# Performance work log

Measured on AMD Instinct MI355X. Metric: run time of the kernel, lower is better.

The kernel has to match this reference:

```python
import jax, jax.numpy as jnp
import numpy as np

HIDDEN = 128
BSZ, C, Q = 8, 512, 64


def setup_inputs() -> dict:
    key = jax.random.key(0)
    k1, k2, k3, k4 = jax.random.split(key, 4)
    h = jax.random.normal(k1, (BSZ, C, HIDDEN), dtype=jnp.float32)
    u = jax.random.normal(k2, (BSZ, Q, HIDDEN), dtype=jnp.float32)
    # torch Linear stores weight as (out, in); xavier-uniform-like init
    lim1 = float(np.sqrt(6.0 / (3 * HIDDEN + HIDDEN)))
    w1 = jax.random.uniform(k3, (HIDDEN, 3 * HIDDEN), jnp.float32, -lim1, lim1)
    b1 = jnp.zeros((HIDDEN,), jnp.float32)
    lim2 = float(np.sqrt(6.0 / (HIDDEN + 1)))
    w2 = jax.random.uniform(k4, (1, HIDDEN), jnp.float32, -lim2, lim2)
    b2 = jnp.zeros((1,), jnp.float32)
    return {"h": h, "u": u, "w1": w1, "b1": b1, "w2": w2, "b2": b2}


def reference(h, u, w1, b1, w2, b2):
    # Decompose l1 weight into blocks acting on [h2, u2, h2*u2] so the
    # (bsz, C, Q, 3*hidden) concat tensor is never materialized.
    hid = h.shape[-1]
    w_h, w_u, w_hu = w1[:, :hid], w1[:, hid:2 * hid], w1[:, 2 * hid:]
    h_proj = jnp.einsum('bcd,kd->bck', h, w_h)          # (b, C, hidden)
    u_proj = jnp.einsum('bqd,kd->bqk', u, w_u)          # (b, Q, hidden)
    hu_proj = jnp.einsum('bcd,bqd,kd->bcqk', h, u, w_hu)  # (b, C, Q, hidden)
    l1 = jax.nn.relu(h_proj[:, :, None, :] + u_proj[:, None, :, :] + hu_proj + b1)
    l2 = jax.nn.relu(jnp.einsum('bcqk,ok->bcqo', l1, w2) + b2)
    out = jnp.squeeze(l2, axis=-1)  # (b, C, Q)
    if out.ndim == 2:  # bsz == 1 case in original
        out = out[None]
    return out
```

## Files before the change

kernel.cpp:

```cpp
#include <hip/hip_runtime.h>
#include <hip/hip_bf16.h>

typedef __bf16 bf16;
typedef __bf16 bf16x4 __attribute__((ext_vector_type(4)));
typedef __bf16 bf16x8 __attribute__((ext_vector_type(8)));
typedef float  f32x4  __attribute__((ext_vector_type(4)));

#define HID   128
#define BSZ   8
#define CDIM  512
#define QDIM  64
#define LDH   136
#define CTILE 128

__global__ __launch_bounds__(256, 2)
void sim_kernel(const float* __restrict__ hptr,
                const float* __restrict__ uptr,
                const float* __restrict__ w1,
                const float* __restrict__ b1,
                const float* __restrict__ w2,
                const float* __restrict__ b2,
                float* __restrict__ out)
{
    __shared__ bf16  weff[HID * LDH];
    __shared__ bf16  hsh[CTILE * LDH];
    __shared__ float ush[HID];
    __shared__ float bias_sh[HID];
    __shared__ float w2sh[HID];

    const int t  = threadIdx.x;
    const int bi = blockIdx.x >> 6;
    const int qi = blockIdx.x & 63;

    const float* uvec = uptr + (bi * QDIM + qi) * HID;

    if (t < HID) {
        ush[t]  = uvec[t];
        w2sh[t] = w2[t];
    }
    __syncthreads();

    {
        const int k     = t >> 1;
        const int dbase = (t & 1) * 64;
        const float* wrow = w1 + k * 384;
        #pragma unroll
        for (int j = 0; j < 16; ++j) {
            const int d = dbase + j * 4;
            float4 wh  = *(const float4*)(wrow + d);
            float4 whu = *(const float4*)(wrow + 256 + d);
            bf16x4 o;
            o[0] = (bf16)(wh.x + ush[d + 0] * whu.x);
            o[1] = (bf16)(wh.y + ush[d + 1] * whu.y);
            o[2] = (bf16)(wh.z + ush[d + 2] * whu.z);
            o[3] = (bf16)(wh.w + ush[d + 3] * whu.w);
            *(bf16x4*)&weff[k * LDH + d] = o;
        }
    }
    if (t < HID) {
        const float* wrow = w1 + t * 384 + 128;
        float acc = 0.f;
        #pragma unroll 8
        for (int d = 0; d < 128; d += 4) {
            float4 wu = *(const float4*)(wrow + d);
            acc += wu.x * ush[d] + wu.y * ush[d + 1] + wu.z * ush[d + 2] + wu.w * ush[d + 3];
        }
        bias_sh[t] = b1[t] + acc;
    }
    __syncthreads();

    const int lane = t & 63;
    const int wv   = t >> 6;
    const int col  = lane & 15;
    const int quad = lane >> 4;

    bf16x8 bfrag[4][8];
    #pragma unroll
    for (int ks = 0; ks < 4; ++ks)
        #pragma unroll
        for (int n = 0; n < 8; ++n)
            bfrag[ks][n] = *(const bf16x8*)&weff[(n * 16 + col) * LDH + ks * 32 + quad * 8];

    float bias_l[8], w2_l[8];
    #pragma unroll
    for (int n = 0; n < 8; ++n) {
        bias_l[n] = bias_sh[n * 16 + col];
        w2_l[n]   = w2sh[n * 16 + col];
    }
    const float b2v = b2[0];

    const float* hbase = hptr + bi * (CDIM * HID);
    float*       obase = out + (bi * CDIM) * QDIM + qi;

    for (int ct = 0; ct < CDIM / CTILE; ++ct) {
        __syncthreads();
        {
            const int c0 = ct * CTILE;
            #pragma unroll
            for (int i = 0; i < 16; ++i) {
                const int flat4 = i * 256 + t;
                const int row   = flat4 >> 5;
                const int c4    = flat4 & 31;
                float4 v = *(const float4*)(hbase + (c0 + row) * HID + c4 * 4);
                bf16x4 o;
                o[0] = (bf16)v.x; o[1] = (bf16)v.y; o[2] = (bf16)v.z; o[3] = (bf16)v.w;
                *(bf16x4*)&hsh[row * LDH + c4 * 4] = o;
            }
        }
        __syncthreads();

        #pragma unroll
        for (int rt = 0; rt < 2; ++rt) {
            f32x4 acc[8];
            #pragma unroll
            for (int n = 0; n < 8; ++n) acc[n] = (f32x4){0.f, 0.f, 0.f, 0.f};

            #pragma unroll
            for (int ks = 0; ks < 4; ++ks) {
                bf16x8 a = *(const bf16x8*)&hsh[(wv * 32 + rt * 16 + col) * LDH + ks * 32 + quad * 8];
                #pragma unroll
                for (int n = 0; n < 8; ++n)
                    acc[n] = __builtin_amdgcn_mfma_f32_16x16x32_bf16(a, bfrag[ks][n], acc[n], 0, 0, 0);
            }

            float s0 = 0.f, s1 = 0.f, s2 = 0.f, s3 = 0.f;
            #pragma unroll
            for (int n = 0; n < 8; ++n) {
                const float bl = bias_l[n], wl = w2_l[n];
                s0 += fmaxf(acc[n][0] + bl, 0.f) * wl;
                s1 += fmaxf(acc[n][1] + bl, 0.f) * wl;
                s2 += fmaxf(acc[n][2] + bl, 0.f) * wl;
                s3 += fmaxf(acc[n][3] + bl, 0.f) * wl;
            }
            #pragma unroll
            for (int off = 1; off < 16; off <<= 1) {
                s0 += __shfl_xor(s0, off, 64);
                s1 += __shfl_xor(s1, off, 64);
                s2 += __shfl_xor(s2, off, 64);
                s3 += __shfl_xor(s3, off, 64);
            }
            if (col < 4) {
                const float sv = col == 0 ? s0 : col == 1 ? s1 : col == 2 ? s2 : s3;
                const int crow = ct * CTILE + wv * 32 + rt * 16 + quad * 4 + col;
                obase[crow * QDIM] = fmaxf(sv + b2v, 0.f);
            }
        }
    }
}

extern "C" void kernel_launch(void* const* d_in, const int* in_sizes, int n_in,
                              void* d_out, int out_size, void* d_ws, size_t ws_size,
                              hipStream_t stream) {
    const float* h  = (const float*)d_in[0];
    const float* u  = (const float*)d_in[1];
    const float* w1 = (const float*)d_in[2];
    const float* b1 = (const float*)d_in[3];
    const float* w2 = (const float*)d_in[4];
    const float* b2 = (const float*)d_in[5];
    float* out = (float*)d_out;

    sim_kernel<<<dim3(BSZ * QDIM), dim3(256), 0, stream>>>(h, u, w1, b1, w2, b2, out);
}
```

Measured before the change: 90.30 us.

## Split into prep kernel for bf16 weights/h and LDS-free main GEMM kernel

Adds a prep kernel that computes the per-(batch,query) effective weights and bias once and converts h to bf16 in a workspace buffer. The main kernel then reads its B fragments and h tiles straight from global memory, with no shared memory staging or block barriers. This removes the per-block w1 and h conversion work, which was repeated across all 64 query blocks. The cost is an extra launch and about 16MB of workspace traffic for the effective weights, and the A tiles now come from global or L2 rather than LDS.

Measured after the change: 95.86 us. 6.2% more time.

```diff
diff --git a/kernel.cpp b/kernel.cpp
--- a/kernel.cpp
+++ b/kernel.cpp
@@ -10,140 +10,162 @@
 #define BSZ   8
 #define CDIM  512
 #define QDIM  64
-#define LDH   136
-#define CTILE 128
+
+#define WEFF_OFF 0u
+#define HBF_OFF  16777216u
+#define BIAS_OFF 17825792u
+
+__global__ __launch_bounds__(256)
+void prep_kernel(const float* __restrict__ hptr,
+                 const float* __restrict__ uptr,
+                 const float* __restrict__ w1,
+                 const float* __restrict__ b1,
+                 char* __restrict__ ws)
+{
+    __shared__ float u_sh[QDIM * 132];
+    __shared__ float w_sh[8 * 388];
+    const int t   = threadIdx.x;
+    const int blk = blockIdx.x;
+
+    if (blk < 128) {
+        const int b  = blk >> 4;
+        const int k0 = (blk & 15) * 8;
+        const float* ub = uptr + b * QDIM * HID;
+
+        #pragma unroll
+        for (int i = 0; i < 8; ++i) {
+            const int f4 = i * 256 + t;
+            const int q  = f4 >> 5, c4 = f4 & 31;
+            float4 v = *(const float4*)(ub + f4 * 4);
+            *(float4*)&u_sh[q * 132 + c4 * 4] = v;
+        }
+        #pragma unroll
+        for (int i = 0; i < 3; ++i) {
+            const int f4 = i * 256 + t;
+            const int r = f4 / 96, c4 = f4 % 96;
+            float4 v = *(const float4*)(w1 + (k0 + r) * 384 + c4 * 4);
+            *(float4*)&w_sh[r * 388 + c4 * 4] = v;
+        }
+        __syncthreads();
+
+        bf16* weff = (bf16*)(ws + WEFF_OFF);
+        #pragma unroll 4
+        for (int i = 0; i < 64; ++i) {
+            const int flat = i * 256 + t;
+            const int row = flat >> 5, ch = flat & 31;
+            const int q = row >> 3, kk = row & 7, d = ch * 4;
+            const float* uu  = &u_sh[q * 132 + d];
+            const float* wh  = &w_sh[kk * 388 + d];
+            const float* whu = &w_sh[kk * 388 + 256 + d];
+            bf16x4 o;
+            o[0] = (bf16)(wh[0] + uu[0] * whu[0]);
+            o[1] = (bf16)(wh[1] + uu[1] * whu[1]);
+            o[2] = (bf16)(wh[2] + uu[2] * whu[2]);
+            o[3] = (bf16)(wh[3] + uu[3] * whu[3]);
+            *(bf16x4*)&weff[(((b * QDIM + q) * HID) + k0 + kk) * HID + d] = o;
+        }
+
+        float* bias = (float*)(ws + BIAS_OFF);
+        #pragma unroll
+        for (int r = 0; r < 2; ++r) {
+            const int p = r * 256 + t;
+            const int q = p >> 3, kk = p & 7;
+            const float* uu = &u_sh[q * 132];
+            const float* wu = &w_sh[kk * 388 + 128];
+            float acc = 0.f;
+            #pragma unroll 8
+            for (int d = 0; d < 128; d += 4) {
+                f32x4 a = *(const f32x4*)&uu[d];
+                f32x4 w = *(const f32x4*)&wu[d];
+                acc += a[0]*w[0] + a[1]*w[1] + a[2]*w[2] + a[3]*w[3];
+            }
+            bias[(b * QDIM + q) * HID + k0 + kk] = b1[k0 + kk] + acc;
+        }
+    } else {
+        const int wg = blk - 128;
+        bf16* hbf = (bf16*)(ws + HBF_OFF);
+        #pragma unroll
+        for (int i = 0; i < 8; ++i) {
+            const int f4 = wg * 2048 + i * 256 + t;
+            float4 v = *(const float4*)(hptr + f4 * 4);
+            bf16x4 o;
+            o[0] = (bf16)v.x; o[1] = (bf16)v.y; o[2] = (bf16)v.z; o[3] = (bf16)v.w;
+            *(bf16x4*)&hbf[f4 * 4] = o;
+        }
+    }
+}
 
 __global__ __launch_bounds__(256, 2)
-void sim_kernel(const float* __restrict__ hptr,
-                const float* __restrict__ uptr,
-                const float* __restrict__ w1,
-                const float* __restrict__ b1,
-                const float* __restrict__ w2,
-                const float* __restrict__ b2,
-                float* __restrict__ out)
+void main_kernel(const char* __restrict__ ws,
+                 const float* __restrict__ w2,
+                 const float* __restrict__ b2,
+                 float* __restrict__ out)
 {
-    __shared__ bf16  weff[HID * LDH];
-    __shared__ bf16  hsh[CTILE * LDH];
-    __shared__ float ush[HID];
-    __shared__ float bias_sh[HID];
-    __shared__ float w2sh[HID];
-
-    const int t  = threadIdx.x;
-    const int bi = blockIdx.x >> 6;
-    const int qi = blockIdx.x & 63;
-
-    const float* uvec = uptr + (bi * QDIM + qi) * HID;
-
-    if (t < HID) {
-        ush[t]  = uvec[t];
-        w2sh[t] = w2[t];
-    }
-    __syncthreads();
-
-    {
-        const int k     = t >> 1;
-        const int dbase = (t & 1) * 64;
-        const float* wrow = w1 + k * 384;
-        #pragma unroll
-        for (int j = 0; j < 16; ++j) {
-            const int d = dbase + j * 4;
-            float4 wh  = *(const float4*)(wrow + d);
-            float4 whu = *(const float4*)(wrow + 256 + d);
-            bf16x4 o;
-            o[0] = (bf16)(wh.x + ush[d + 0] * whu.x);
-            o[1] = (bf16)(wh.y + ush[d + 1] * whu.y);
-            o[2] = (bf16)(wh.z + ush[d + 2] * whu.z);
-            o[3] = (bf16)(wh.w + ush[d + 3] * whu.w);
-            *(bf16x4*)&weff[k * LDH + d] = o;
-        }
-    }
-    if (t < HID) {
-        const float* wrow = w1 + t * 384 + 128;
-        float acc = 0.f;
-        #pragma unroll 8
-        for (int d = 0; d < 128; d += 4) {
-            float4 wu = *(const float4*)(wrow + d);
-            acc += wu.x * ush[d] + wu.y * ush[d + 1] + wu.z * ush[d + 2] + wu.w * ush[d + 3];
-        }
-        bias_sh[t] = b1[t] + acc;
-    }
-    __syncthreads();
-
+    const int t    = threadIdx.x;
+    const int bi   = blockIdx.x >> 6;
+    const int qi   = blockIdx.x & 63;
     const int lane = t & 63;
     const int wv   = t >> 6;
     const int col  = lane & 15;
     const int quad = lane >> 4;
+
+    const bf16*  weff = (const bf16*)(ws + WEFF_OFF) + (size_t)(bi * QDIM + qi) * (HID * HID);
+    const float* bias = (const float*)(ws + BIAS_OFF) + (bi * QDIM + qi) * HID;
+    const bf16*  hbf  = (const bf16*)(ws + HBF_OFF) + (size_t)bi * CDIM * HID;
 
     bf16x8 bfrag[4][8];
     #pragma unroll
     for (int ks = 0; ks < 4; ++ks)
         #pragma unroll
         for (int n = 0; n < 8; ++n)
-            bfrag[ks][n] = *(const bf16x8*)&weff[(n * 16 + col) * LDH + ks * 32 + quad * 8];
+            bfrag[ks][n] = *(const bf16x8*)&weff[(n * 16 + col) * HID + ks * 32 + quad * 8];
 
     float bias_l[8], w2_l[8];
     #pragma unroll
     for (int n = 0; n < 8; ++n) {
-        bias_l[n] = bias_sh[n * 16 + col];
-        w2_l[n]   = w2sh[n * 16 + col];
+        bias_l[n] = bias[n * 16 + col];
+        w2_l[n]   = w2[n * 16 + col];
     }
     const float b2v = b2[0];
 
-    const float* hbase = hptr + bi * (CDIM * HID);
-    float*       obase = out + (bi * CDIM) * QDIM + qi;
+    float* obase = out + (bi * CDIM) * QDIM + qi;
 
-    for (int ct = 0; ct < CDIM / CTILE; ++ct) {
-        __syncthreads();
-        {
-            const int c0 = ct * CTILE;
-            #pragma unroll
-            for (int i = 0; i < 16; ++i) {
-                const int flat4 = i * 256 + t;
-                const int row   = flat4 >> 5;
-                const int c4    = flat4 & 31;
-                float4 v = *(const float4*)(hbase + (c0 + row) * HID + c4 * 4);
-                bf16x4 o;
-                o[0] = (bf16)v.x; o[1] = (bf16)v.y; o[2] = (bf16)v.z; o[3] = (bf16)v.w;
-                *(bf16x4*)&hsh[row * LDH + c4 * 4] = o;
-            }
-        }
-        __syncthreads();
+    #pragma unroll 2
+    for (int rt = 0; rt < 8; ++rt) {
+        const int c0 = wv * 128 + rt * 16;
+
+        f32x4 acc[8];
+        #pragma unroll
+        for (int n = 0; n < 8; ++n) acc[n] = (f32x4){0.f, 0.f, 0.f, 0.f};
 
         #pragma unroll
-        for (int rt = 0; rt < 2; ++rt) {
-            f32x4 acc[8];
+        for (int ks = 0; ks < 4; ++ks) {
+            bf16x8 a = *(const bf16x8*)&hbf[(c0 + col) * HID + ks * 32 + quad * 8];
             #pragma unroll
-            for (int n = 0; n < 8; ++n) acc[n] = (f32x4){0.f, 0.f, 0.f, 0.f};
+            for (int n = 0; n < 8; ++n)
+                acc[n] = __builtin_amdgcn_mfma_f32_16x16x32_bf16(a, bfrag[ks][n], acc[n], 0, 0, 0);
+        }
 
-            #pragma unroll
-            for (int ks = 0; ks < 4; ++ks) {
-                bf16x8 a = *(const bf16x8*)&hsh[(wv * 32 + rt * 16 + col) * LDH + ks * 32 + quad * 8];
-                #pragma unroll
-                for (int n = 0; n < 8; ++n)
-                    acc[n] = __builtin_amdgcn_mfma_f32_16x16x32_bf16(a, bfrag[ks][n], acc[n], 0, 0, 0);
-            }
-
-            float s0 = 0.f, s1 = 0.f, s2 = 0.f, s3 = 0.f;
-            #pragma unroll
-            for (int n = 0; n < 8; ++n) {
-                const float bl = bias_l[n], wl = w2_l[n];
-                s0 += fmaxf(acc[n][0] + bl, 0.f) * wl;
-                s1 += fmaxf(acc[n][1] + bl, 0.f) * wl;
-                s2 += fmaxf(acc[n][2] + bl, 0.f) * wl;
-                s3 += fmaxf(acc[n][3] + bl, 0.f) * wl;
-            }
-            #pragma unroll
-            for (int off = 1; off < 16; off <<= 1) {
-                s0 += __shfl_xor(s0, off, 64);
-                s1 += __shfl_xor(s1, off, 64);
-                s2 += __shfl_xor(s2, off, 64);
-                s3 += __shfl_xor(s3, off, 64);
-            }
-            if (col < 4) {
-                const float sv = col == 0 ? s0 : col == 1 ? s1 : col == 2 ? s2 : s3;
-                const int crow = ct * CTILE + wv * 32 + rt * 16 + quad * 4 + col;
-                obase[crow * QDIM] = fmaxf(sv + b2v, 0.f);
-            }
+        float s0 = 0.f, s1 = 0.f, s2 = 0.f, s3 = 0.f;
+        #pragma unroll
+        for (int n = 0; n < 8; ++n) {
+            const float bl = bias_l[n], wl = w2_l[n];
+            s0 += fmaxf(acc[n][0] + bl, 0.f) * wl;
+            s1 += fmaxf(acc[n][1] + bl, 0.f) * wl;
+            s2 += fmaxf(acc[n][2] + bl, 0.f) * wl;
+            s3 += fmaxf(acc[n][3] + bl, 0.f) * wl;
+        }
+        #pragma unroll
+        for (int off = 1; off < 16; off <<= 1) {
+            s0 += __shfl_xor(s0, off, 64);
+            s1 += __shfl_xor(s1, off, 64);
+            s2 += __shfl_xor(s2, off, 64);
+            s3 += __shfl_xor(s3, off, 64);
+        }
+        if (col < 4) {
+            const float sv = col == 0 ? s0 : col == 1 ? s1 : col == 2 ? s2 : s3;
+            const int crow = c0 + quad * 4 + col;
+            obase[crow * QDIM] = fmaxf(sv + b2v, 0.f);
         }
     }
 }
@@ -158,6 +180,8 @@
     const float* w2 = (const float*)d_in[4];
     const float* b2 = (const float*)d_in[5];
     float* out = (float*)d_out;
+    char* ws = (char*)d_ws;
 
-    sim_kernel<<<dim3(BSZ * QDIM), dim3(256), 0, stream>>>(h, u, w1, b1, w2, b2, out);
+    prep_kernel<<<dim3(192), dim3(256), 0, stream>>>(h, u, w1, b1, ws);
+    main_kernel<<<dim3(BSZ * QDIM), dim3(256), 0, stream>>>(ws, w2, b2, out);
 }
```

## Load h fragments directly from global into MFMA registers, drop LDS staging

Applied to the files above, without the earlier changes.

Removes the shared-memory staging of the h tile and its block-wide barriers. Each wave now reads its own 128 rows of h straight from global memory as float4 pairs, converts them to bf16 in registers and feeds the MFMA. The aim is to cut LDS traffic and __syncthreads stalls and to free LDS for occupancy. The cost is global loads that are less coalesced (each lane reads 32 bytes from a different row), which rely on cache hits since h is shared across the 64 q-blocks.

Result: slower. 96.51 us (+6.9%).

```diff
diff --git a/kernel.cpp b/kernel.cpp
--- a/kernel.cpp
+++ b/kernel.cpp
@@ -11,7 +11,6 @@
 #define CDIM  512
 #define QDIM  64
 #define LDH   136
-#define CTILE 128
 
 __global__ __launch_bounds__(256, 2)
 void sim_kernel(const float* __restrict__ hptr,
@@ -23,7 +22,6 @@
                 float* __restrict__ out)
 {
     __shared__ bf16  weff[HID * LDH];
-    __shared__ bf16  hsh[CTILE * LDH];
     __shared__ float ush[HID];
     __shared__ float bias_sh[HID];
     __shared__ float w2sh[HID];
@@ -92,58 +90,48 @@
     const float* hbase = hptr + bi * (CDIM * HID);
     float*       obase = out + (bi * CDIM) * QDIM + qi;
 
-    for (int ct = 0; ct < CDIM / CTILE; ++ct) {
-        __syncthreads();
-        {
-            const int c0 = ct * CTILE;
-            #pragma unroll
-            for (int i = 0; i < 16; ++i) {
-                const int flat4 = i * 256 + t;
-                const int row   = flat4 >> 5;
-                const int c4    = flat4 & 31;
-                float4 v = *(const float4*)(hbase + (c0 + row) * HID + c4 * 4);
-                bf16x4 o;
-                o[0] = (bf16)v.x; o[1] = (bf16)v.y; o[2] = (bf16)v.z; o[3] = (bf16)v.w;
-                *(bf16x4*)&hsh[row * LDH + c4 * 4] = o;
-            }
-        }
-        __syncthreads();
+    #pragma unroll 2
+    for (int rt = 0; rt < 8; ++rt) {
+        const int c0 = wv * 128 + rt * 16;
+        const float* arow = hbase + (c0 + col) * HID;
+
+        f32x4 acc[8];
+        #pragma unroll
+        for (int n = 0; n < 8; ++n) acc[n] = (f32x4){0.f, 0.f, 0.f, 0.f};
 
         #pragma unroll
-        for (int rt = 0; rt < 2; ++rt) {
-            f32x4 acc[8];
+        for (int ks = 0; ks < 4; ++ks) {
+            const float* ap = arow + ks * 32 + quad * 8;
+            float4 v0 = *(const float4*)(ap);
+            float4 v1 = *(const float4*)(ap + 4);
+            bf16x8 a;
+            a[0] = (bf16)v0.x; a[1] = (bf16)v0.y; a[2] = (bf16)v0.z; a[3] = (bf16)v0.w;
+            a[4] = (bf16)v1.x; a[5] = (bf16)v1.y; a[6] = (bf16)v1.z; a[7] = (bf16)v1.w;
             #pragma unroll
-            for (int n = 0; n < 8; ++n) acc[n] = (f32x4){0.f, 0.f, 0.f, 0.f};
+            for (int n = 0; n < 8; ++n)
+                acc[n] = __builtin_amdgcn_mfma_f32_16x16x32_bf16(a, bfrag[ks][n], acc[n], 0, 0, 0);
+        }
 
-            #pragma unroll
-            for (int ks = 0; ks < 4; ++ks) {
-                bf16x8 a = *(const bf16x8*)&hsh[(wv * 32 + rt * 16 + col) * LDH + ks * 32 + quad * 8];
-                #pragma unroll
-                for (int n = 0; n < 8; ++n)
-                    acc[n] = __builtin_amdgcn_mfma_f32_16x16x32_bf16(a, bfrag[ks][n], acc[n], 0, 0, 0);
-            }
-
-            float s0 = 0.f, s1 = 0.f, s2 = 0.f, s3 = 0.f;
-            #pragma unroll
-            for (int n = 0; n < 8; ++n) {
-                const float bl = bias_l[n], wl = w2_l[n];
-                s0 += fmaxf(acc[n][0] + bl, 0.f) * wl;
-                s1 += fmaxf(acc[n][1] + bl, 0.f) * wl;
-                s2 += fmaxf(acc[n][2] + bl, 0.f) * wl;
-                s3 += fmaxf(acc[n][3] + bl, 0.f) * wl;
-            }
-            #pragma unroll
-            for (int off = 1; off < 16; off <<= 1) {
-                s0 += __shfl_xor(s0, off, 64);
-                s1 += __shfl_xor(s1, off, 64);
-                s2 += __shfl_xor(s2, off, 64);
-                s3 += __shfl_xor(s3, off, 64);
-            }
-            if (col < 4) {
-                const float sv = col == 0 ? s0 : col == 1 ? s1 : col == 2 ? s2 : s3;
-                const int crow = ct * CTILE + wv * 32 + rt * 16 + quad * 4 + col;
-                obase[crow * QDIM] = fmaxf(sv + b2v, 0.f);
-            }
+        float s0 = 0.f, s1 = 0.f, s2 = 0.f, s3 = 0.f;
+        #pragma unroll
+        for (int n = 0; n < 8; ++n) {
+            const float bl = bias_l[n], wl = w2_l[n];
+            s0 += fmaxf(acc[n][0] + bl, 0.f) * wl;
+            s1 += fmaxf(acc[n][1] + bl, 0.f) * wl;
+            s2 += fmaxf(acc[n][2] + bl, 0.f) * wl;
+            s3 += fmaxf(acc[n][3] + bl, 0.f) * wl;
+        }
+        #pragma unroll
+        for (int off = 1; off < 16; off <<= 1) {
+            s0 += __shfl_xor(s0, off, 64);
+            s1 += __shfl_xor(s1, off, 64);
+            s2 += __shfl_xor(s2, off, 64);
+            s3 += __shfl_xor(s3, off, 64);
+        }
+        if (col < 4) {
+            const float sv = col == 0 ? s0 : col == 1 ? s1 : col == 2 ? s2 : s3;
+            const int crow = c0 + quad * 4 + col;
+            obase[crow * QDIM] = fmaxf(sv + b2v, 0.f);
         }
     }
 }
```
